# Performance work log

Measured on AMD Instinct MI355X. Metric: run time of the kernel, lower is better.

## Reference

```python
import jax, jax.numpy as jnp
import numpy as np

NUM_HEADS = 16
THETA = 10000.0


def setup_inputs() -> dict:
    key = jax.random.key(0)
    k1, k2, k3, k4 = jax.random.split(key, 4)
    B, T, D = 2, 2048, 1024
    x = jax.random.normal(k1, (B, T, D), dtype=jnp.float32)
    token_positions = jnp.sort(
        jax.random.randint(k2, (B, T), 0, 2048), axis=-1
    ).astype(jnp.int32)
    sigma_qkv = float(np.sqrt(2.0 / (D + 3 * D)))
    sigma_out = float(np.sqrt(2.0 / (D + D)))
    W_qkv = jax.random.normal(k3, (3 * D, D), dtype=jnp.float32) * sigma_qkv
    W_out = jax.random.normal(k4, (D, D), dtype=jnp.float32) * sigma_out
    return {"x": x, "token_positions": token_positions, "W_qkv": W_qkv, "W_out": W_out}


def _apply_rope(t, cos, sin):
    # t: [B, H, T, d_k]; cos/sin: [B, T, d_k//2]
    B, H, T, dk = t.shape
    t2 = t.reshape(B, H, T, dk // 2, 2)
    te, to = t2[..., 0], t2[..., 1]
    c = cos[:, None]  # [B, 1, T, dk//2]
    s = sin[:, None]
    ye = te * c - to * s
    yo = to * c + te * s
    return jnp.stack([ye, yo], axis=-1).reshape(B, H, T, dk)


def reference(x, token_positions, W_qkv, W_out):
    B, T, D = x.shape
    H = NUM_HEADS
    dk = D // H

    # fused QKV projection: [B, T, 3D] -> split (three, h, d) on last dim
    qkv = jnp.einsum("btd,od->bto", x, W_qkv).reshape(B, T, 3, H, dk)
    qkv = jnp.transpose(qkv, (2, 0, 3, 1, 4))  # [3, B, H, T, dk]
    q, k, v = qkv[0], qkv[1], qkv[2]

    # RoPE angles from token positions
    n = jnp.arange(dk // 2, dtype=jnp.float32)
    inv_freq = THETA ** (-2.0 * n / dk)  # [dk//2]
    angles = token_positions.astype(jnp.float32)[..., None] * inv_freq  # [B, T, dk//2]
    cos, sin = jnp.cos(angles), jnp.sin(angles)
    q = _apply_rope(q, cos, sin)
    k = _apply_rope(k, cos, sin)

    # causal scaled dot-product attention
    scores = jnp.einsum("bhid,bhjd->bhij", q, k) / jnp.sqrt(jnp.float32(dk))
    causal = jnp.tril(jnp.ones((T, T), dtype=bool))
    scores = jnp.where(causal, scores, -jnp.inf)
    probs = jax.nn.softmax(scores, axis=-1)
    attn = jnp.einsum("bhij,bhjd->bhid", probs, v)  # [B, H, T, dk]

    concat = jnp.transpose(attn, (0, 2, 1, 3)).reshape(B, T, D)
    return jnp.einsum("btd,od->bto", concat, W_out)
```

## Files before the change

kernel.cpp:

```cpp
#include <hip/hip_runtime.h>
#include <hip/hip_bf16.h>
#include <cmath>

#define T_SEQ 2048
#define D_MODEL 1024
#define NHEAD 16
#define DK 64

typedef short bf16x8 __attribute__((ext_vector_type(8)));
typedef float f32x4 __attribute__((ext_vector_type(4)));
typedef float f32x16 __attribute__((ext_vector_type(16)));
typedef unsigned uint2v __attribute__((ext_vector_type(2)));

union U8 { unsigned u[4]; bf16x8 v; };

#define VMCNT(n) asm volatile("s_waitcnt vmcnt(" #n ")" ::: "memory")
#define BAR() __builtin_amdgcn_s_barrier()
#define SFENCE() __builtin_amdgcn_sched_barrier(0)

__device__ __forceinline__ short f2b(float f) {
    unsigned u = __builtin_bit_cast(unsigned, f);
    unsigned r = (u + 0x7FFFu + ((u >> 16) & 1u)) >> 16;
    return (short)r;
}

__device__ __forceinline__ void gll16(const void* g, void* l) {
    __builtin_amdgcn_global_load_lds(
        (__attribute__((address_space(1))) void*)g,
        (__attribute__((address_space(3))) void*)l, 16, 0, 0);
}

__device__ __forceinline__ unsigned pkbf16(float a, float b) {
    unsigned r;
    asm("v_cvt_pk_bf16_f32 %0, %1, %2" : "=v"(r) : "v"(a), "v"(b));
    return r;
}
__device__ __forceinline__ void pl32swap(unsigned& a, unsigned& b) {
    uint2v r = __builtin_amdgcn_permlane32_swap(a, b, false, false);
    a = r.x; b = r.y;
}

__global__ __launch_bounds__(256) void cvt_all(const float* __restrict__ x,
                                               const float* __restrict__ wq,
                                               const float* __restrict__ wo,
                                               const int* __restrict__ pos,
                                               short* __restrict__ xb,
                                               short* __restrict__ wqb,
                                               short* __restrict__ wob,
                                               float* __restrict__ ct,
                                               float* __restrict__ st) {
    int i = blockIdx.x * 256 + threadIdx.x;
    if (i >= 1048576) {
        int j = i - 1048576;
        int bt = j >> 5, n = j & 31;
        float p = (float)pos[bt];
        float invf = expf((float)n * (-2.0f / (float)DK) * 9.210340371976184f);
        float s, c;
        sincosf(p * invf, &s, &c);
        ct[j] = c; st[j] = s;
        return;
    }
    const float* src;
    short* dst;
    int srcoff, c;
    if (i < 524288) {
        c = i;
        int tile = c >> 9, cc = c & 511;
        int kblk = cc >> 7, row = cc & 127;
        int rb = tile >> 5, kb = tile & 31;
        srcoff = (rb * 128 + row) * D_MODEL + kb * 32 + kblk * 8;
        src = x; dst = xb;
    } else if (i < 917504) {
        c = i - 524288;
        int tile = c >> 9, cc = c & 511;
        int kblk = cc >> 7, row = cc & 127;
        int rb = tile >> 5, kb = tile & 31;
        srcoff = (rb * 128 + row) * D_MODEL + kb * 32 + kblk * 8;
        src = wq; dst = wqb;
    } else {
        c = i - 917504;
        int tile = c >> 8, cc = c & 255;
        int kblk = cc >> 6, row = cc & 63;
        int nb = tile >> 5, kb = tile & 31;
        srcoff = (nb * 64 + row) * D_MODEL + kb * 32 + kblk * 8;
        src = wo; dst = wob;
    }
    float4 a = *reinterpret_cast<const float4*>(src + srcoff);
    float4 b = *reinterpret_cast<const float4*>(src + srcoff + 4);
    bf16x8 v;
    v[0] = f2b(a.x); v[1] = f2b(a.y); v[2] = f2b(a.z); v[3] = f2b(a.w);
    v[4] = f2b(b.x); v[5] = f2b(b.y); v[6] = f2b(b.z); v[7] = f2b(b.w);
    reinterpret_cast<bf16x8*>(dst)[c] = v;
}

__global__ __launch_bounds__(256, 3) void gemm_qkv(const short* __restrict__ xb,
                                                   const short* __restrict__ wb,
                                                   const float* __restrict__ ct,
                                                   const float* __restrict__ st,
                                                   short* __restrict__ Qo,
                                                   short* __restrict__ Ko,
                                                   short* __restrict__ Vt) {
    __shared__ short SM[3][8192];
    const int tid = threadIdx.x;
    const int w = tid >> 6, l = tid & 63, lg = l >> 4, li = l & 15;
    const int wr = w >> 1, wc = w & 1;
    const int bn = blockIdx.x * 128, bm = blockIdx.y * 128;

    const short* pA = xb + (size_t)blockIdx.y * 32 * 4096 + (w * 128 + l) * 8;
    const short* pB = wb + (size_t)blockIdx.x * 32 * 4096 + (w * 128 + l) * 8;

    f32x4 zero = {0.f, 0.f, 0.f, 0.f};
    f32x4 acc[4][4];
#pragma unroll
    for (int m = 0; m < 4; ++m)
#pragma unroll
        for (int n = 0; n < 4; ++n) acc[m][n] = zero;

#define GSTAGE(buf, t_)                                               \
    do {                                                              \
        const size_t ko = (size_t)(t_) * 4096;                        \
        gll16(pA + ko,       &SM[buf][w * 1024]);                     \
        gll16(pA + ko + 512, &SM[buf][w * 1024 + 512]);               \
        gll16(pB + ko,       &SM[buf][4096 + w * 1024]);              \
        gll16(pB + ko + 512, &SM[buf][4096 + w * 1024 + 512]);        \
    } while (0)

    GSTAGE(0, 0);
    GSTAGE(1, 1);

    for (int t = 0; t < 32; ++t) {
        if (t < 31) { VMCNT(4); } else { VMCNT(0); }
        BAR();
        SFENCE();
        if (t + 2 < 32) GSTAGE((t + 2) % 3, t + 2);
        const short* Ac = &SM[t % 3][0];
        const short* Bc = &SM[t % 3][4096];
        bf16x8 a[4], b[4];
#pragma unroll
        for (int m = 0; m < 4; ++m)
            a[m] = *reinterpret_cast<const bf16x8*>(&Ac[lg * 1024 + (wr * 64 + m * 16 + li) * 8]);
#pragma unroll
        for (int n = 0; n < 4; ++n)
            b[n] = *reinterpret_cast<const bf16x8*>(&Bc[lg * 1024 + (wc * 64 + n * 16 + li) * 8]);
        __builtin_amdgcn_s_setprio(1);
#pragma unroll
        for (int m = 0; m < 4; ++m)
#pragma unroll
            for (int n = 0; n < 4; ++n)
                acc[m][n] = __builtin_amdgcn_mfma_f32_16x16x32_bf16(a[m], b[n], acc[m][n], 0, 0, 0);
        __builtin_amdgcn_s_setprio(0);
    }
#undef GSTAGE

    const int which = bn >> 10;
    const int h = ((bn >> 6) + wc) & 15;
    if (which == 2) {
        __syncthreads();
        short* scr = &SM[0][0] + w * 4096;
#pragma unroll
        for (int n = 0; n < 4; ++n)
#pragma unroll
            for (int m = 0; m < 4; ++m)
#pragma unroll
                for (int rp = 0; rp < 2; ++rp) {
                    int d = n * 16 + li;
                    int t64 = m * 16 + lg * 4 + rp * 2;
                    unsigned pk = pkbf16(acc[m][n][rp * 2], acc[m][n][rp * 2 + 1]);
                    *reinterpret_cast<unsigned*>(
                        (char*)scr + ((d * 128 + t64 * 2) ^ ((d & 7) << 4))) = pk;
                }
        const int mi0 = bm + wr * 64;
        const int b0 = mi0 >> 11, t0 = mi0 & (T_SEQ - 1);
        const int kvt = t0 >> 6;
        short* vbase = Vt + ((size_t)(b0 * NHEAD + h) * 32 + kvt) * 4096;
        const int ch = l >> 3;
#pragma unroll
        for (int db = 0; db < 8; ++db) {
            int d = db * 8 + (l & 7);
            bf16x8 v = *reinterpret_cast<const bf16x8*>(
                (char*)scr + ((d * 128 + ch * 16) ^ ((d & 7) << 4)));
            *reinterpret_cast<bf16x8*>(vbase + ch * 512 + d * 8) = v;
        }
    } else {
#pragma unroll
        for (int n = 0; n < 4; ++n) {
            const int d = n * 16 + li;
#pragma unroll
            for (int m = 0; m < 4; ++m)
#pragma unroll
                for (int r = 0; r < 4; ++r) {
                    const int mi = bm + wr * 64 + m * 16 + lg * 4 + r;
                    const int b_ = mi >> 11, tt = mi & (T_SEQ - 1);
                    float v = acc[m][n][r];
                    float vp = __shfl_xor(v, 1);
                    int nn = n * 8 + (li >> 1);
                    float c = ct[(size_t)mi * 32 + nn];
                    float s = st[(size_t)mi * 32 + nn];
                    float o = (d & 1) ? (v * c + vp * s) : (v * c - vp * s);
                    if (which == 0) o *= 0.18033688011112042f;
                    short* dst = (which == 0) ? Qo : Ko;
                    dst[((size_t)((b_ * NHEAD + h) * T_SEQ + tt)) * DK + d] = f2b(o);
                }
        }
    }
}

__global__ __launch_bounds__(256, 2) void attn(const short* __restrict__ Q,
                                               const short* __restrict__ K,
                                               const short* __restrict__ Vt,
                                               short* __restrict__ Cc) {
    const int bid = blockIdx.x;
    const int ii = bid & 255, rhalf = bid >> 8;
    const int bh = ii & 31;
    const int qt = rhalf ? 15 - (ii >> 5) : (ii >> 5);

    const int tid = threadIdx.x;
    const int w = tid >> 6, l = tid & 63;
    const int l31 = l & 31, hi = l >> 5, hi4 = hi * 4, hi8 = hi * 8;
    const int q0w = qt * 128 + w * 32;
    const int Tw = (q0w + 32 + 63) >> 6;

    const short* Qh = Q + (size_t)bh * T_SEQ * DK;
    const short* Kh = K + (size_t)bh * T_SEQ * DK;
    const short* Vh = Vt + (size_t)bh * 32 * 4096;

    bf16x8 qf[4];
#pragma unroll
    for (int ks = 0; ks < 4; ++ks)
        qf[ks] = *reinterpret_cast<const bf16x8*>(&Qh[(size_t)(q0w + l31) * DK + ks * 16 + hi8]);

    const f32x16 Z16 = {0.f,0.f,0.f,0.f,0.f,0.f,0.f,0.f,0.f,0.f,0.f,0.f,0.f,0.f,0.f,0.f};
    f32x16 o0 = Z16, o1 = Z16;
    float m = -3.0e38f;
    float lsum = 0.f;

    const short* kp0 = Kh + (size_t)l31 * DK + hi8;
    const short* kp1 = Kh + (size_t)(32 + l31) * DK + hi8;

#define KVLOAD(kk_, vv_, t_)                                                           \
    do {                                                                               \
        const size_t ko = (size_t)(t_) * 64 * DK;                                      \
        _Pragma("unroll")                                                              \
        for (int ks = 0; ks < 4; ++ks) {                                               \
            kk_[ks]     = *reinterpret_cast<const bf16x8*>(kp0 + ko + ks * 16);        \
            kk_[4 + ks] = *reinterpret_cast<const bf16x8*>(kp1 + ko + ks * 16);        \
        }                                                                              \
        const short* vt = Vh + (size_t)(t_) * 4096;                                    \
        vv_[0] = *reinterpret_cast<const bf16x8*>(vt + (0 + hi) * 512 + l31 * 8);      \
        vv_[1] = *reinterpret_cast<const bf16x8*>(vt + (2 + hi) * 512 + l31 * 8);      \
        vv_[2] = *reinterpret_cast<const bf16x8*>(vt + (0 + hi) * 512 + 256 + l31 * 8); \
        vv_[3] = *reinterpret_cast<const bf16x8*>(vt + (2 + hi) * 512 + 256 + l31 * 8); \
        vv_[4] = *reinterpret_cast<const bf16x8*>(vt + (4 + hi) * 512 + l31 * 8);      \
        vv_[5] = *reinterpret_cast<const bf16x8*>(vt + (6 + hi) * 512 + l31 * 8);      \
        vv_[6] = *reinterpret_cast<const bf16x8*>(vt + (4 + hi) * 512 + 256 + l31 * 8); \
        vv_[7] = *reinterpret_cast<const bf16x8*>(vt + (6 + hi) * 512 + 256 + l31 * 8); \
    } while (0)

#define COMPUTE(t_, kk_, vv_)                                                          \
    do {                                                                               \
        const int n0 = (t_) * 64;                                                      \
        f32x16 s0 = Z16, s1 = Z16;                                                     \
        __builtin_amdgcn_s_setprio(1);                                                 \
        _Pragma("unroll")                                                              \
        for (int ks = 0; ks < 4; ++ks) {                                               \
            s0 = __builtin_amdgcn_mfma_f32_32x32x16_bf16(kk_[ks],     qf[ks], s0, 0, 0, 0); \
            s1 = __builtin_amdgcn_mfma_f32_32x32x16_bf16(kk_[4 + ks], qf[ks], s1, 0, 0, 0); \
        }                                                                              \
        __builtin_amdgcn_s_setprio(0);                                                 \
        float p[32];                                                                   \
        _Pragma("unroll")                                                              \
        for (int r = 0; r < 16; ++r) { p[r] = s0[r]; p[16 + r] = s1[r]; }              \
        if (n0 + 64 > q0w) {                                                           \
            const int qrel = q0w + l31 - n0;                                           \
            _Pragma("unroll")                                                          \
            for (int r = 0; r < 16; ++r) {                                             \
                const int kvm = (r & 3) + 8 * (r >> 2) + hi4;                          \
                if (kvm > qrel) p[r] = -3.0e38f;                                       \
                if (kvm + 32 > qrel) p[16 + r] = -3.0e38f;                             \
            }                                                                          \
        }                                                                              \
        float t16[16];                                                                 \
        _Pragma("unroll")                                                              \
        for (int r = 0; r < 16; ++r) t16[r] = fmaxf(p[r], p[16 + r]);                  \
        _Pragma("unroll")                                                              \
        for (int d = 8; d >= 1; d >>= 1)                                               \
            _Pragma("unroll")                                                          \
            for (int r = 0; r < 8; ++r)                                                \
                if (r < d) t16[r] = fmaxf(t16[r], t16[r + d]);                         \
        float tmax = fmaxf(t16[0], __shfl_xor(t16[0], 32));                            \
        if (__any(tmax > m + 8.0f)) {                                                  \
            float mnew = fmaxf(m, tmax);                                               \
            float alpha = __builtin_amdgcn_exp2f(m - mnew);                            \
            m = mnew;                                                                  \
            _Pragma("unroll")                                                          \
            for (int r = 0; r < 16; ++r) {                                             \
                float ar = __shfl(alpha, (r & 3) + 8 * (r >> 2) + hi4);                \
                o0[r] *= ar; o1[r] *= ar;                                              \
            }                                                                          \
            lsum *= alpha;                                                             \
        }                                                                              \
        _Pragma("unroll")                                                              \
        for (int r = 0; r < 32; ++r) p[r] = __builtin_amdgcn_exp2f(p[r] - m);          \
        float a16[16];                                                                 \
        _Pragma("unroll")                                                              \
        for (int r = 0; r < 16; ++r) a16[r] = p[r] + p[16 + r];                        \
        _Pragma("unroll")                                                              \
        for (int d = 8; d >= 1; d >>= 1)                                               \
            _Pragma("unroll")                                                          \
            for (int r = 0; r < 8; ++r)                                                \
                if (r < d) a16[r] += a16[r + d];                                       \
        lsum += a16[0] + __shfl_xor(a16[0], 32);                                       \
        __builtin_amdgcn_s_setprio(1);                                                 \
        _Pragma("unroll")                                                              \
        for (int kb = 0; kb < 2; ++kb) {                                               \
            unsigned pk0 = pkbf16(p[kb * 16 + 0],  p[kb * 16 + 1]);                    \
            unsigned pk1 = pkbf16(p[kb * 16 + 2],  p[kb * 16 + 3]);                    \
            unsigned pk2 = pkbf16(p[kb * 16 + 4],  p[kb * 16 + 5]);                    \
            unsigned pk3 = pkbf16(p[kb * 16 + 6],  p[kb * 16 + 7]);                    \
            unsigned pk4 = pkbf16(p[kb * 16 + 8],  p[kb * 16 + 9]);                    \
            unsigned pk5 = pkbf16(p[kb * 16 + 10], p[kb * 16 + 11]);                   \
            unsigned pk6 = pkbf16(p[kb * 16 + 12], p[kb * 16 + 13]);                   \
            unsigned pk7 = pkbf16(p[kb * 16 + 14], p[kb * 16 + 15]);                   \
            pl32swap(pk0, pk2); pl32swap(pk1, pk3);                                    \
            pl32swap(pk4, pk6); pl32swap(pk5, pk7);                                    \
            U8 f0, f1;                                                                 \
            f0.u[0] = pk0; f0.u[1] = pk1; f0.u[2] = pk2; f0.u[3] = pk3;                \
            f1.u[0] = pk4; f1.u[1] = pk5; f1.u[2] = pk6; f1.u[3] = pk7;                \
            o0 = __builtin_amdgcn_mfma_f32_32x32x16_bf16(f0.v, vv_[kb * 4 + 0], o0, 0, 0, 0); \
            o0 = __builtin_amdgcn_mfma_f32_32x32x16_bf16(f1.v, vv_[kb * 4 + 1], o0, 0, 0, 0); \
            o1 = __builtin_amdgcn_mfma_f32_32x32x16_bf16(f0.v, vv_[kb * 4 + 2], o1, 0, 0, 0); \
            o1 = __builtin_amdgcn_mfma_f32_32x32x16_bf16(f1.v, vv_[kb * 4 + 3], o1, 0, 0, 0); \
        }                                                                              \
        __builtin_amdgcn_s_setprio(0);                                                 \
    } while (0)

    bf16x8 kA[8], vA[8], kB[8], vB[8];

    KVLOAD(kA, vA, 0);
    if (1 < Tw) KVLOAD(kB, vB, 1);

    for (int t = 0; t < Tw; t += 2) {
        COMPUTE(t, kA, vA);
        if (t + 2 < Tw) KVLOAD(kA, vA, t + 2);
        if (t + 1 < Tw) {
            COMPUTE(t + 1, kB, vB);
            if (t + 3 < Tw) KVLOAD(kB, vB, t + 3);
        }
    }
#undef COMPUTE
#undef KVLOAD

    const int b = bh >> 4, h = bh & 15;
    const float linv = 1.0f / lsum;
#pragma unroll
    for (int r = 0; r < 16; ++r) {
        const int qoff = (r & 3) + 8 * (r >> 2) + hi4;
        float inv = __shfl(linv, qoff);
        const int mg = b * T_SEQ + q0w + qoff;
        const int mb = mg >> 7, row = mg & 127;
        const int kblk = l31 >> 3, el = l & 7;
        Cc[((size_t)(mb * 32 + h * 2 + 0)) * 4096 + kblk * 1024 + row * 8 + el] = f2b(o0[r] * inv);
        Cc[((size_t)(mb * 32 + h * 2 + 1)) * 4096 + kblk * 1024 + row * 8 + el] = f2b(o1[r] * inv);
    }
}

__global__ __launch_bounds__(256, 3) void gemm_out(const short* __restrict__ ab,
                                                   const short* __restrict__ wb,
                                                   float* __restrict__ out) {
    __shared__ short SM[3][6144];
    const int tid = threadIdx.x;
    const int w = tid >> 6, l = tid & 63, lg = l >> 4, li = l & 15;
    const int wr = w >> 1, wc = w & 1;
    const int bn = blockIdx.x * 64, bm = blockIdx.y * 128;

    const short* pA = ab + (size_t)blockIdx.y * 32 * 4096 + (w * 128 + l) * 8;
    const short* pB = wb + (size_t)blockIdx.x * 32 * 2048 + (w * 64 + l) * 8;

    f32x4 zero = {0.f, 0.f, 0.f, 0.f};
    f32x4 acc[4][2];
#pragma unroll
    for (int m = 0; m < 4; ++m)
#pragma unroll
        for (int n = 0; n < 2; ++n) acc[m][n] = zero;

#define OSTAGE(buf, t_)                                                  \
    do {                                                                 \
        gll16(pA + (size_t)(t_) * 4096,       &SM[buf][w * 1024]);       \
        gll16(pA + (size_t)(t_) * 4096 + 512, &SM[buf][w * 1024 + 512]); \
        gll16(pB + (size_t)(t_) * 2048,       &SM[buf][4096 + w * 512]); \
    } while (0)

    OSTAGE(0, 0);
    OSTAGE(1, 1);

    for (int t = 0; t < 32; ++t) {
        if (t < 31) { VMCNT(3); } else { VMCNT(0); }
        BAR();
        SFENCE();
        if (t + 2 < 32) OSTAGE((t + 2) % 3, t + 2);
        const short* Ac = &SM[t % 3][0];
        const short* Bc = &SM[t % 3][4096];
        bf16x8 a[4], b[2];
#pragma unroll
        for (int m = 0; m < 4; ++m)
            a[m] = *reinterpret_cast<const bf16x8*>(&Ac[lg * 1024 + (wr * 64 + m * 16 + li) * 8]);
#pragma unroll
        for (int n = 0; n < 2; ++n)
            b[n] = *reinterpret_cast<const bf16x8*>(&Bc[lg * 512 + (wc * 32 + n * 16 + li) * 8]);
        __builtin_amdgcn_s_setprio(1);
#pragma unroll
        for (int m = 0; m < 4; ++m)
#pragma unroll
            for (int n = 0; n < 2; ++n)
                acc[m][n] = __builtin_amdgcn_mfma_f32_16x16x32_bf16(a[m], b[n], acc[m][n], 0, 0, 0);
        __builtin_amdgcn_s_setprio(0);
    }
#undef OSTAGE

#pragma unroll
    for (int m = 0; m < 4; ++m)
#pragma unroll
        for (int n = 0; n < 2; ++n)
#pragma unroll
            for (int r = 0; r < 4; ++r) {
                const int mi = bm + wr * 64 + m * 16 + lg * 4 + r;
                out[(size_t)mi * D_MODEL + bn + wc * 32 + n * 16 + li] = acc[m][n][r];
            }
}

extern "C" void kernel_launch(void* const* d_in, const int* in_sizes, int n_in,
                              void* d_out, int out_size, void* d_ws, size_t ws_size,
                              hipStream_t stream) {
    const float* x    = (const float*)d_in[0];
    const int*   pos  = (const int*)d_in[1];
    const float* wqkv = (const float*)d_in[2];
    const float* wout = (const float*)d_in[3];
    float* out = (float*)d_out;

    char* ws = (char*)d_ws;
    size_t off = 0;
    short* xb  = (short*)(ws + off); off += (size_t)4096 * 1024 * 2;
    short* wqb = (short*)(ws + off); off += (size_t)3072 * 1024 * 2;
    short* wob = (short*)(ws + off); off += (size_t)1024 * 1024 * 2;
    short* Q   = (short*)(ws + off); off += (size_t)32 * 2048 * 64 * 2;
    short* Kb  = (short*)(ws + off); off += (size_t)32 * 2048 * 64 * 2;
    short* Vt  = (short*)(ws + off); off += (size_t)32 * 32 * 4096 * 2;
    off += 4096;
    short* Cc  = (short*)(ws + off); off += (size_t)4096 * 1024 * 2;
    float* ct  = (float*)(ws + off); off += (size_t)4096 * 32 * 4;
    float* st  = (float*)(ws + off); off += (size_t)4096 * 32 * 4;

    cvt_all<<<4608, 256, 0, stream>>>(x, wqkv, wout, pos, xb, wqb, wob, ct, st);
    gemm_qkv<<<dim3(24, 32), 256, 0, stream>>>(xb, wqb, ct, st, Q, Kb, Vt);
    attn<<<512, 256, 0, stream>>>(Q, Kb, Vt, Cc);
    gemm_out<<<dim3(16, 32), 256, 0, stream>>>(Cc, wob, out);
}
```

Baseline: 113.2 us.

## Split KV tiles across two waves per query block and merge partials in LDS

```diff
diff --git a/kernel.cpp b/kernel.cpp
--- a/kernel.cpp
+++ b/kernel.cpp
@@ -205,20 +205,23 @@
     }
 }
 
-__global__ __launch_bounds__(256, 2) void attn(const short* __restrict__ Q,
+__global__ __launch_bounds__(128, 4) void attn(const short* __restrict__ Q,
                                                const short* __restrict__ K,
                                                const short* __restrict__ Vt,
                                                short* __restrict__ Cc) {
+    __shared__ float Osh[32][64];
+    __shared__ float MLs[2][32];
+
     const int bid = blockIdx.x;
-    const int ii = bid & 255, rhalf = bid >> 8;
-    const int bh = ii & 31;
-    const int qt = rhalf ? 15 - (ii >> 5) : (ii >> 5);
+    const int bh = bid & 31;
+    const int qg = 63 - (bid >> 5);
+    const int q0 = qg * 32;
 
     const int tid = threadIdx.x;
-    const int w = tid >> 6, l = tid & 63;
+    const int w = tid >> 6;
+    const int l = tid & 63;
     const int l31 = l & 31, hi = l >> 5, hi4 = hi * 4, hi8 = hi * 8;
-    const int q0w = qt * 128 + w * 32;
-    const int Tw = (q0w + 32 + 63) >> 6;
+    const int Tw = (q0 + 32 + 63) >> 6;
 
     const short* Qh = Q + (size_t)bh * T_SEQ * DK;
     const short* Kh = K + (size_t)bh * T_SEQ * DK;
@@ -227,7 +230,7 @@
     bf16x8 qf[4];
 #pragma unroll
     for (int ks = 0; ks < 4; ++ks)
-        qf[ks] = *reinterpret_cast<const bf16x8*>(&Qh[(size_t)(q0w + l31) * DK + ks * 16 + hi8]);
+        qf[ks] = *reinterpret_cast<const bf16x8*>(&Qh[(size_t)(q0 + l31) * DK + ks * 16 + hi8]);
 
     const f32x16 Z16 = {0.f,0.f,0.f,0.f,0.f,0.f,0.f,0.f,0.f,0.f,0.f,0.f,0.f,0.f,0.f,0.f};
     f32x16 o0 = Z16, o1 = Z16;
@@ -270,8 +273,8 @@
         float p[32];                                                                   \
         _Pragma("unroll")                                                              \
         for (int r = 0; r < 16; ++r) { p[r] = s0[r]; p[16 + r] = s1[r]; }              \
-        if (n0 + 64 > q0w) {                                                           \
-            const int qrel = q0w + l31 - n0;                                           \
+        if (n0 + 64 > q0) {                                                            \
+            const int qrel = q0 + l31 - n0;                                            \
             _Pragma("unroll")                                                          \
             for (int r = 0; r < 16; ++r) {                                             \
                 const int kvm = (r & 3) + 8 * (r >> 2) + hi4;                          \
@@ -336,31 +339,52 @@
 
     bf16x8 kA[8], vA[8], kB[8], vB[8];
 
-    KVLOAD(kA, vA, 0);
-    if (1 < Tw) KVLOAD(kB, vB, 1);
-
-    for (int t = 0; t < Tw; t += 2) {
+    if (w < Tw)     KVLOAD(kA, vA, w);
+    if (w + 2 < Tw) KVLOAD(kB, vB, w + 2);
+
+    for (int t = w; t < Tw; t += 4) {
         COMPUTE(t, kA, vA);
-        if (t + 2 < Tw) KVLOAD(kA, vA, t + 2);
-        if (t + 1 < Tw) {
-            COMPUTE(t + 1, kB, vB);
-            if (t + 3 < Tw) KVLOAD(kB, vB, t + 3);
+        if (t + 4 < Tw) KVLOAD(kA, vA, t + 4);
+        if (t + 2 < Tw) {
+            COMPUTE(t + 2, kB, vB);
+            if (t + 6 < Tw) KVLOAD(kB, vB, t + 6);
         }
     }
 #undef COMPUTE
 #undef KVLOAD
 
-    const int b = bh >> 4, h = bh & 15;
-    const float linv = 1.0f / lsum;
-#pragma unroll
-    for (int r = 0; r < 16; ++r) {
-        const int qoff = (r & 3) + 8 * (r >> 2) + hi4;
-        float inv = __shfl(linv, qoff);
-        const int mg = b * T_SEQ + q0w + qoff;
-        const int mb = mg >> 7, row = mg & 127;
-        const int kblk = l31 >> 3, el = l & 7;
-        Cc[((size_t)(mb * 32 + h * 2 + 0)) * 4096 + kblk * 1024 + row * 8 + el] = f2b(o0[r] * inv);
-        Cc[((size_t)(mb * 32 + h * 2 + 1)) * 4096 + kblk * 1024 + row * 8 + el] = f2b(o1[r] * inv);
+    if (w == 1) {
+#pragma unroll
+        for (int r = 0; r < 16; ++r) {
+            const int qoff = (r & 3) + 8 * (r >> 2) + hi4;
+            Osh[qoff][l31] = o0[r];
+            Osh[qoff][32 + l31] = o1[r];
+        }
+        if (l < 32) { MLs[0][l] = m; MLs[1][l] = lsum; }
+    }
+    __syncthreads();
+    if (w == 0) {
+        const float m2 = MLs[0][l31];
+        const float l2 = MLs[1][l31];
+        const float M = fmaxf(m, m2);
+        const float a1 = __builtin_amdgcn_exp2f(m - M);
+        const float a2 = __builtin_amdgcn_exp2f(m2 - M);
+        const float linv = 1.0f / (lsum * a1 + l2 * a2);
+        const int b = bh >> 4, h = bh & 15;
+#pragma unroll
+        for (int r = 0; r < 16; ++r) {
+            const int qoff = (r & 3) + 8 * (r >> 2) + hi4;
+            const float a1r = __shfl(a1, qoff);
+            const float a2r = __shfl(a2, qoff);
+            const float ir  = __shfl(linv, qoff);
+            const float f0 = (o0[r] * a1r + Osh[qoff][l31] * a2r) * ir;
+            const float f1 = (o1[r] * a1r + Osh[qoff][32 + l31] * a2r) * ir;
+            const int mg = b * T_SEQ + q0 + qoff;
+            const int mb = mg >> 7, row = mg & 127;
+            const int kblk = l31 >> 3, el = l & 7;
+            Cc[((size_t)(mb * 32 + h * 2 + 0)) * 4096 + kblk * 1024 + row * 8 + el] = f2b(f0);
+            Cc[((size_t)(mb * 32 + h * 2 + 1)) * 4096 + kblk * 1024 + row * 8 + el] = f2b(f1);
+        }
     }
 }
 
@@ -452,6 +476,6 @@
 
     cvt_all<<<4608, 256, 0, stream>>>(x, wqkv, wout, pos, xb, wqb, wob, ct, st);
     gemm_qkv<<<dim3(24, 32), 256, 0, stream>>>(xb, wqb, ct, st, Q, Kb, Vt);
-    attn<<<512, 256, 0, stream>>>(Q, Kb, Vt, Cc);
+    attn<<<2048, 128, 0, stream>>>(Q, Kb, Vt, Cc);
     gemm_out<<<dim3(16, 32), 256, 0, stream>>>(Cc, wob, out);
 }
```

Result: slower. 254.0 us (+124.4%).

## Split attention into single-wave blocks and swizzle GEMM block order for XCDs

Applied to the files above, without the earlier changes.

```diff
diff --git a/kernel.cpp b/kernel.cpp
--- a/kernel.cpp
+++ b/kernel.cpp
@@ -104,10 +104,12 @@
     const int tid = threadIdx.x;
     const int w = tid >> 6, l = tid & 63, lg = l >> 4, li = l & 15;
     const int wr = w >> 1, wc = w & 1;
-    const int bn = blockIdx.x * 128, bm = blockIdx.y * 128;
-
-    const short* pA = xb + (size_t)blockIdx.y * 32 * 4096 + (w * 128 + l) * 8;
-    const short* pB = wb + (size_t)blockIdx.x * 32 * 4096 + (w * 128 + l) * 8;
+    const int swz = (blockIdx.x & 7) * 96 + (blockIdx.x >> 3);
+    const int bxi = swz % 24, byi = swz / 24;
+    const int bn = bxi * 128, bm = byi * 128;
+
+    const short* pA = xb + (size_t)byi * 32 * 4096 + (w * 128 + l) * 8;
+    const short* pB = wb + (size_t)bxi * 32 * 4096 + (w * 128 + l) * 8;
 
     f32x4 zero = {0.f, 0.f, 0.f, 0.f};
     f32x4 acc[4][4];
@@ -205,20 +207,18 @@
     }
 }
 
-__global__ __launch_bounds__(256, 2) void attn(const short* __restrict__ Q,
-                                               const short* __restrict__ K,
-                                               const short* __restrict__ Vt,
-                                               short* __restrict__ Cc) {
+__global__ __launch_bounds__(64, 3) void attn(const short* __restrict__ Q,
+                                              const short* __restrict__ K,
+                                              const short* __restrict__ Vt,
+                                              short* __restrict__ Cc) {
     const int bid = blockIdx.x;
-    const int ii = bid & 255, rhalf = bid >> 8;
-    const int bh = ii & 31;
-    const int qt = rhalf ? 15 - (ii >> 5) : (ii >> 5);
-
-    const int tid = threadIdx.x;
-    const int w = tid >> 6, l = tid & 63;
+    const int bh = bid & 31;
+    const int qg = 63 - (bid >> 5);
+    const int q0 = qg * 32;
+    const int Tw = (q0 + 32 + 63) >> 6;
+
+    const int l = threadIdx.x;
     const int l31 = l & 31, hi = l >> 5, hi4 = hi * 4, hi8 = hi * 8;
-    const int q0w = qt * 128 + w * 32;
-    const int Tw = (q0w + 32 + 63) >> 6;
 
     const short* Qh = Q + (size_t)bh * T_SEQ * DK;
     const short* Kh = K + (size_t)bh * T_SEQ * DK;
@@ -227,7 +227,7 @@
     bf16x8 qf[4];
 #pragma unroll
     for (int ks = 0; ks < 4; ++ks)
-        qf[ks] = *reinterpret_cast<const bf16x8*>(&Qh[(size_t)(q0w + l31) * DK + ks * 16 + hi8]);
+        qf[ks] = *reinterpret_cast<const bf16x8*>(&Qh[(size_t)(q0 + l31) * DK + ks * 16 + hi8]);
 
     const f32x16 Z16 = {0.f,0.f,0.f,0.f,0.f,0.f,0.f,0.f,0.f,0.f,0.f,0.f,0.f,0.f,0.f,0.f};
     f32x16 o0 = Z16, o1 = Z16;
@@ -270,8 +270,8 @@
         float p[32];                                                                   \
         _Pragma("unroll")                                                              \
         for (int r = 0; r < 16; ++r) { p[r] = s0[r]; p[16 + r] = s1[r]; }              \
-        if (n0 + 64 > q0w) {                                                           \
-            const int qrel = q0w + l31 - n0;                                           \
+        if (n0 + 64 > q0) {                                                            \
+            const int qrel = q0 + l31 - n0;                                            \
             _Pragma("unroll")                                                          \
             for (int r = 0; r < 16; ++r) {                                             \
                 const int kvm = (r & 3) + 8 * (r >> 2) + hi4;                          \
@@ -356,7 +356,7 @@
     for (int r = 0; r < 16; ++r) {
         const int qoff = (r & 3) + 8 * (r >> 2) + hi4;
         float inv = __shfl(linv, qoff);
-        const int mg = b * T_SEQ + q0w + qoff;
+        const int mg = b * T_SEQ + q0 + qoff;
         const int mb = mg >> 7, row = mg & 127;
         const int kblk = l31 >> 3, el = l & 7;
         Cc[((size_t)(mb * 32 + h * 2 + 0)) * 4096 + kblk * 1024 + row * 8 + el] = f2b(o0[r] * inv);
@@ -371,10 +371,12 @@
     const int tid = threadIdx.x;
     const int w = tid >> 6, l = tid & 63, lg = l >> 4, li = l & 15;
     const int wr = w >> 1, wc = w & 1;
-    const int bn = blockIdx.x * 64, bm = blockIdx.y * 128;
-
-    const short* pA = ab + (size_t)blockIdx.y * 32 * 4096 + (w * 128 + l) * 8;
-    const short* pB = wb + (size_t)blockIdx.x * 32 * 2048 + (w * 64 + l) * 8;
+    const int swz = (blockIdx.x & 7) * 64 + (blockIdx.x >> 3);
+    const int bxi = swz % 16, byi = swz / 16;
+    const int bn = bxi * 64, bm = byi * 128;
+
+    const short* pA = ab + (size_t)byi * 32 * 4096 + (w * 128 + l) * 8;
+    const short* pB = wb + (size_t)bxi * 32 * 2048 + (w * 64 + l) * 8;
 
     f32x4 zero = {0.f, 0.f, 0.f, 0.f};
     f32x4 acc[4][2];
@@ -451,7 +453,7 @@
     float* st  = (float*)(ws + off); off += (size_t)4096 * 32 * 4;
 
     cvt_all<<<4608, 256, 0, stream>>>(x, wqkv, wout, pos, xb, wqb, wob, ct, st);
-    gemm_qkv<<<dim3(24, 32), 256, 0, stream>>>(xb, wqb, ct, st, Q, Kb, Vt);
-    attn<<<512, 256, 0, stream>>>(Q, Kb, Vt, Cc);
-    gemm_out<<<dim3(16, 32), 256, 0, stream>>>(Cc, wob, out);
-}
+    gemm_qkv<<<768, 256, 0, stream>>>(xb, wqb, ct, st, Q, Kb, Vt);
+    attn<<<2048, 64, 0, stream>>>(Q, Kb, Vt, Cc);
+    gemm_out<<<512, 256, 0, stream>>>(Cc, wob, out);
+}
```

New measurement: 227.5 us. +100.9%, slower.
